# Kernel optimization log

Measured on AMD Instinct MI355X. Metric: run time of the kernel, lower is better.

## Reference

```python
import jax, jax.numpy as jnp
import numpy as np

D_MODEL = 128
SEQ_LEN = 2048
WINDOW = 64
BATCH = 32


def setup_inputs() -> dict:
    key = jax.random.key(0)
    ks = jax.random.split(key, 6)
    scale = 1.0 / np.sqrt(D_MODEL)
    return {
        "x": jax.random.normal(ks[0], (BATCH, D_MODEL, SEQ_LEN), dtype=jnp.float32),
        "Wq": jax.random.normal(ks[1], (D_MODEL, D_MODEL), dtype=jnp.float32) * scale,
        "bq": jnp.zeros((D_MODEL,), dtype=jnp.float32),
        "Wk": jax.random.normal(ks[2], (D_MODEL, D_MODEL), dtype=jnp.float32) * scale,
        "bk": jnp.zeros((D_MODEL,), dtype=jnp.float32),
        "Wv": jax.random.normal(ks[3], (D_MODEL, D_MODEL), dtype=jnp.float32) * scale,
        "bv": jnp.zeros((D_MODEL,), dtype=jnp.float32),
        "Wo": jax.random.normal(ks[4], (D_MODEL, D_MODEL), dtype=jnp.float32) * scale,
        "bo": jnp.zeros((D_MODEL,), dtype=jnp.float32),
        "pos_bias": jax.random.normal(ks[5], (SEQ_LEN, SEQ_LEN), dtype=jnp.float32) * 0.02,
    }


def reference(x, Wq, bq, Wk, bk, Wv, bv, Wo, bo, pos_bias):
    # x: [N, C, L] -> [N, L, C]  (in_proj Rearrange)
    xt = jnp.swapaxes(x, 1, 2)
    L = xt.shape[1]

    q = xt @ Wq + bq  # [N, L, d]
    k = xt @ Wk + bk
    v = xt @ Wv + bv

    # AFT-Local positional bias: w_{t,t'} = pos_bias if |t-t'| < s else 0
    idx = jnp.arange(L)
    local_mask = (jnp.abs(idx[:, None] - idx[None, :]) < WINDOW).astype(xt.dtype)
    pb = pos_bias[:L, :L] * local_mask  # [L, L]

    # numerically stable exponentials (AFT paper / labml formulation)
    exp_k = jnp.exp(k - jnp.max(k, axis=1, keepdims=True))          # [N, L, d]
    exp_pb = jnp.exp(pb - jnp.max(pb, axis=1, keepdims=True))       # [L, L]

    num = jnp.einsum('ij,njd->nid', exp_pb, exp_k * v)  # [N, L, d]
    den = jnp.einsum('ij,njd->nid', exp_pb, exp_k)      # [N, L, d]

    y = jax.nn.sigmoid(q) * num / den
    out = y @ Wo + bo  # output projection

    # out_proj Rearrange: [N, L, C] -> [N, C, L]
    return jnp.swapaxes(out, 1, 2)
```

## Files before the change

### kernel.cpp

```cpp
#include <hip/hip_runtime.h>
#include <hip/hip_bf16.h>
#include <math.h>

#define NB 32
#define DM 128
#define SL 2048
#define WIN 64
#define NT  (SL / 16)
#define PADF 4
#define PADB 6
#define NTP (NT + PADF + PADB)
#define YST 132
#define OST 68
#define NSEG 64

typedef __attribute__((ext_vector_type(8))) short bf16x8;
typedef __attribute__((ext_vector_type(8))) unsigned short u16x8;
typedef __attribute__((ext_vector_type(4))) float f32x4;
typedef __attribute__((ext_vector_type(4))) unsigned int u32x4;

__device__ inline ushort bf16_rne(float f) {
    union { float f; unsigned u; } v; v.f = f;
    unsigned u = v.u;
    return (ushort)((u + 0x7FFFu + ((u >> 16) & 1u)) >> 16);
}
__device__ inline float bf16_to_f(ushort h) {
    union { unsigned u; float f; } v; v.u = ((unsigned)h) << 16;
    return v.f;
}
__device__ inline unsigned pk_bf16(float a, float b) {
    union { __hip_bfloat162 h; unsigned u; } v;
    v.h = __float22bfloat162_rn(make_float2(a, b));
    return v.u;
}


__global__ __launch_bounds__(512) void setup_kernel(
    const float* __restrict__ Wq, const float* __restrict__ Wk,
    const float* __restrict__ Wv, const float* __restrict__ Wo,
    const float* __restrict__ pos_bias,
    ushort* __restrict__ Wh, ushort* __restrict__ Wl,
    ushort* __restrict__ WB)
{
    const int b = blockIdx.x;
    const int tid = threadIdx.x;
    if (b < 128) {
        const int id = b;
        const int mat = id >> 5;
        const int ct = (id & 31) >> 2, ks = id & 3;
        const int lane = tid >> 3, j = tid & 7;
        const int k = ks * 32 + (lane >> 4) * 8 + j;
        const int col = ct * 16 + (lane & 15);
        const float* W = (mat == 0) ? Wq : ((mat == 1) ? Wk : ((mat == 2) ? Wv : Wo));
        float w = W[k * DM + col];
        ushort h = bf16_rne(w);
        Wh[(size_t)id * 512 + tid] = h;
        Wl[(size_t)id * 512 + tid] = bf16_rne(w - bf16_to_f(h));
    } else {
        const int idx = b - 128;
        const int it = idx >> 1;
        const int half = idx & 1;
        const int i0 = it * 16;
        const int tend = half * 1280 + 1280;
        for (int t = half * 1280 + tid; t < tend; t += 512) {
            const int ks = t >> 9;
            const int lane = (t >> 3) & 63;
            const int jj = t & 7;
            const int m = lane & 15;
            const int k = ks * 32 + ((lane >> 4) << 3) + jj;
            const int i = i0 + m;
            const int j = i0 - 64 + k;
            const int rel = k - 64 - m;
            float val = 0.f;
            if (rel > -WIN && rel < WIN && j >= 0 && j < SL)
                val = __expf(pos_bias[(size_t)i * SL + j]) - 1.f;
            WB[(size_t)it * 2560 + t] = bf16_rne(val);
        }
    }
}

__global__ __launch_bounds__(512, 6) void qkv_kernel(
    const float* __restrict__ x,
    const ushort* __restrict__ Wh, const ushort* __restrict__ Wl,
    const float* __restrict__ bq, const float* __restrict__ bk,
    const float* __restrict__ bv,
    ushort* __restrict__ sqT, ushort* __restrict__ ekTF, ushort* __restrict__ ekvTF,
    float* __restrict__ Pk, float* __restrict__ Pkv)
{
    __shared__ ushort Ah[32 * 128];
    __shared__ ushort Al[32 * 128];
    const int n = blockIdx.y, bx = blockIdx.x, l0 = bx * 32;
    const int tid = threadIdx.x;
    const int wave = tid >> 6;
    const int lane = tid & 63;

    if (bx < 10) {
        const int jt_p = (bx < PADF) ? bx : (NT + bx);
        const size_t zb = ((size_t)n * NTP + jt_p) * 2048 + (size_t)tid * 4;
        ushort4 z; z.x = 0; z.y = 0; z.z = 0; z.w = 0;
        *(ushort4*)&ekTF [zb] = z;
        *(ushort4*)&ekvTF[zb] = z;
    }

    {
        const int lo = tid & 31;
        const int cq = tid >> 5;
        const int l  = l0 + lo;
        const int c0 = cq * 8;
        float xv[8];
        #pragma unroll
        for (int u = 0; u < 8; ++u)
            xv[u] = x[((size_t)n * DM + c0 + u) * SL + l];
        unsigned xb[8];
        #pragma unroll
        for (int u = 0; u < 8; ++u) xb[u] = __float_as_uint(xv[u]);
        unsigned hv32[4], lv32[4];
        #pragma unroll
        for (int p = 0; p < 4; ++p) {
            hv32[p] = (xb[2 * p] >> 16) | (xb[2 * p + 1] & 0xFFFF0000u);
            const float r0 = xv[2 * p]     - __uint_as_float(xb[2 * p]     & 0xFFFF0000u);
            const float r1 = xv[2 * p + 1] - __uint_as_float(xb[2 * p + 1] & 0xFFFF0000u);
            lv32[p] = pk_bf16(r0, r1);
        }
        const int lt = lo >> 4, m = lo & 15;
        const int ks = cq >> 2, oct = cq & 3;
        const int idx = ((lt * 4 + ks) * 64 + oct * 16 + m) * 8;
        *(uint4*)&Ah[idx] = make_uint4(hv32[0], hv32[1], hv32[2], hv32[3]);
        *(uint4*)&Al[idx] = make_uint4(lv32[0], lv32[1], lv32[2], lv32[3]);
    }
    __syncthreads();

    const int dcol = lane & 15;
    const int d = wave * 16 + dcol;

    f32x4 acc[3][2];
    {
        const float b0 = bq[d], b1 = bk[d], b2 = bv[d];
        #pragma unroll
        for (int lt = 0; lt < 2; ++lt) {
            acc[0][lt] = (f32x4){b0, b0, b0, b0};
            acc[1][lt] = (f32x4){b1, b1, b1, b1};
            acc[2][lt] = (f32x4){b2, b2, b2, b2};
        }
    }

    const bf16x8* WhV = (const bf16x8*)Wh;
    const bf16x8* WlV = (const bf16x8*)Wl;
    #pragma unroll
    for (int ks = 0; ks < 4; ++ks) {
        bf16x8 bh[3], bl[3];
        #pragma unroll
        for (int m = 0; m < 3; ++m) {
            const int fi = ((m * 8 + wave) * 4 + ks) * 64 + lane;
            bh[m] = WhV[fi];
            bl[m] = WlV[fi];
        }
        #pragma unroll
        for (int lt = 0; lt < 2; ++lt) {
            const bf16x8 ah = *(const bf16x8*)&Ah[((lt * 4 + ks) * 64 + lane) * 8];
            const bf16x8 al = *(const bf16x8*)&Al[((lt * 4 + ks) * 64 + lane) * 8];
            #pragma unroll
            for (int m = 0; m < 3; ++m) {
                acc[m][lt] = __builtin_amdgcn_mfma_f32_16x16x32_bf16(
                    ah, bh[m], acc[m][lt], 0, 0, 0);
                acc[m][lt] = __builtin_amdgcn_mfma_f32_16x16x32_bf16(
                    al, bh[m], acc[m][lt], 0, 0, 0);
                acc[m][lt] = __builtin_amdgcn_mfma_f32_16x16x32_bf16(
                    ah, bl[m], acc[m][lt], 0, 0, 0);
            }
        }
    }

    const int lrow0 = (lane >> 4) * 4;
    float psk = 0.f, pskv = 0.f;
    #pragma unroll
    for (int lt = 0; lt < 2; ++lt) {
        const f32x4 q4 = acc[0][lt];
        const f32x4 k4 = acc[1][lt];
        const f32x4 v4 = acc[2][lt];
        float e[4], z[4];
        unsigned su[4];
        #pragma unroll
        for (int r = 0; r < 4; ++r) {
            e[r] = __expf(k4[r]);
            z[r] = e[r] * v4[r];
            const float s = fminf(__builtin_amdgcn_rcpf(1.f + __expf(-q4[r])), 1.f);
            su[r] = (unsigned)(s * 65535.f + 0.5f);
            psk  += e[r];
            pskv += z[r];
        }
        const int jt = bx * 2 + lt;
        const size_t tb = ((size_t)n * NTP + PADF + jt) * 2048
                        + (size_t)d * 16 + lrow0;
        const size_t sb = ((size_t)n * NT + jt) * 2048
                        + (size_t)d * 16 + lrow0;
        *(uint2*)&ekTF [tb] = make_uint2(pk_bf16(e[0], e[1]), pk_bf16(e[2], e[3]));
        *(uint2*)&ekvTF[tb] = make_uint2(pk_bf16(z[0], z[1]), pk_bf16(z[2], z[3]));
        *(uint2*)&sqT  [sb] = make_uint2(su[0] | (su[1] << 16), su[2] | (su[3] << 16));
    }
    {
        float a = psk, b = pskv;
        a += __shfl_xor(a, 16, 64); a += __shfl_xor(a, 32, 64);
        b += __shfl_xor(b, 16, 64); b += __shfl_xor(b, 32, 64);
        if (lane < 16) {
            const size_t o = ((size_t)n * NSEG + bx) * DM + d;
            Pk [o] = a;
            Pkv[o] = b;
        }
    }
}

__global__ __launch_bounds__(256, 4) void band_out_kernel(
    const ushort* __restrict__ ekTF, const ushort* __restrict__ ekvTF,
    const ushort* __restrict__ WB,
    const float* __restrict__ Pk, const float* __restrict__ Pkv,
    const ushort* __restrict__ sqT,
    const ushort* __restrict__ Wh, const ushort* __restrict__ Wl,
    const float* __restrict__ bo, float* __restrict__ out)
{
    __shared__ __align__(16) union {
        float ylds[64 * YST];
        float ot[128 * OST];
        float red[8][DM];
    } u;
    __shared__ float SkL[DM], SkvL[DM];

    const int bid = blockIdx.x;
    const int xcd = bid & 7;
    const int slot = bid >> 3;
    const int nsub = slot >> 5;
    const int itg  = slot & 31;
    const int n = xcd * 4 + nsub;
    const int wave = threadIdx.x >> 6;
    const int lane = threadIdx.x & 63;
    const int it = itg * 4 + wave;
    const int l0 = itg * 64;

    const int dcol = lane & 15;
    const int jgrp8 = (lane >> 4) << 3;

    const bf16x8* WBv = (const bf16x8*)(WB + (size_t)it * 2560);
    bf16x8 aWB[5];
    #pragma unroll
    for (int ks = 0; ks < 5; ++ks) aWB[ks] = WBv[ks * 64 + lane];

    {
        const int tid = threadIdx.x;
        const int q = tid & 31;
        const int g = tid >> 5;
        const float* P = (g < 4) ? Pk : Pkv;
        const int s0 = (g & 3) * 16;
        f32x4 a4 = (f32x4){0.f, 0.f, 0.f, 0.f};
        #pragma unroll
        for (int s = 0; s < 16; ++s) {
            const f32x4 v = *(const f32x4*)&P[((size_t)n * NSEG + s0 + s) * DM + q * 4];
            a4 += v;
        }
        *(f32x4*)&u.red[g][q * 4] = a4;
    }
    __syncthreads();
    {
        const int tid = threadIdx.x;
        if (tid < 128)
            SkL[tid]  = u.red[0][tid] + u.red[1][tid] + u.red[2][tid] + u.red[3][tid];
        else {
            const int dd = tid - 128;
            SkvL[dd] = u.red[4][dd] + u.red[5][dd] + u.red[6][dd] + u.red[7][dd];
        }
    }
    __syncthreads();

    const size_t lsel = (size_t)(lane >> 5) * 2048 + (size_t)((lane >> 4) & 1) * 8
                      + (size_t)dcol * 16;
    size_t tb[5];
    #pragma unroll
    for (int ks = 0; ks < 5; ++ks)
        tb[ks] = ((size_t)n * NTP + it + 2 * ks) * 2048 + lsel;

    const int irow0 = (lane >> 4) << 2;
    const size_t sgb = ((size_t)n * NT + it) * 2048 + irow0;

    #pragma unroll
    for (int dt = 0; dt < 8; ++dt) {
        const int d = dt * 16 + dcol;
        const float sk = SkL[d];
        const float sv = SkvL[d];
        f32x4 den = (f32x4){sk, sk, sk, sk};
        f32x4 num = (f32x4){sv, sv, sv, sv};
        #pragma unroll
        for (int ks = 0; ks < 5; ++ks) {
            const size_t rbase = tb[ks] + (size_t)dt * 256;
            const bf16x8 bden = *(const bf16x8*)(ekTF  + rbase);
            const bf16x8 bnum = *(const bf16x8*)(ekvTF + rbase);
            den = __builtin_amdgcn_mfma_f32_16x16x32_bf16(aWB[ks], bden, den, 0, 0, 0);
            num = __builtin_amdgcn_mfma_f32_16x16x32_bf16(aWB[ks], bnum, num, 0, 0, 0);
        }
        const ushort4 s4 = *(const ushort4*)&sqT[sgb + (size_t)d * 16];
        float sf[4];
        sf[0] = (float)s4.x; sf[1] = (float)s4.y;
        sf[2] = (float)s4.z; sf[3] = (float)s4.w;
        #pragma unroll
        for (int r = 0; r < 4; ++r) {
            const float s = sf[r] * (1.f / 65535.f);
            const float y = s * num[r] * __builtin_amdgcn_rcpf(den[r]);
            u.ylds[(wave * 16 + irow0 + r) * YST + d] = y;
        }
    }

    bf16x8 yh[4], yl[4];
    {
        const int arow = wave * 16 + (lane & 15);
        #pragma unroll
        for (int ks = 0; ks < 4; ++ks) {
            const int base = arow * YST + ks * 32 + jgrp8;
            const float4 a0 = *(const float4*)&u.ylds[base];
            const float4 a1 = *(const float4*)&u.ylds[base + 4];
            float af[8];
            af[0] = a0.x; af[1] = a0.y; af[2] = a0.z; af[3] = a0.w;
            af[4] = a1.x; af[5] = a1.y; af[6] = a1.z; af[7] = a1.w;
            unsigned ab[8];
            #pragma unroll
            for (int t = 0; t < 8; ++t) ab[t] = __float_as_uint(af[t]);
            unsigned hw[4], lw[4];
            #pragma unroll
            for (int p = 0; p < 4; ++p) {
                hw[p] = (ab[2 * p] >> 16) | (ab[2 * p + 1] & 0xFFFF0000u);
                const float r0 = af[2 * p]     - __uint_as_float(ab[2 * p]     & 0xFFFF0000u);
                const float r1 = af[2 * p + 1] - __uint_as_float(ab[2 * p + 1] & 0xFFFF0000u);
                lw[p] = pk_bf16(r0, r1);
            }
            union { u32x4 w; bf16x8 b; } ch, cl;
            ch.w = (u32x4){hw[0], hw[1], hw[2], hw[3]};
            cl.w = (u32x4){lw[0], lw[1], lw[2], lw[3]};
            yh[ks] = ch.b;
            yl[ks] = cl.b;
        }
    }
    __syncthreads();

    const bf16x8* WhV = (const bf16x8*)Wh;
    const bf16x8* WlV = (const bf16x8*)Wl;
    #pragma unroll
    for (int ct = 0; ct < 8; ++ct) {
        const float b0 = bo[ct * 16 + dcol];
        f32x4 acc = (f32x4){b0, b0, b0, b0};
        #pragma unroll
        for (int ks = 0; ks < 4; ++ks) {
            const int fi = ((24 + ct) * 4 + ks) * 64 + lane;
            const bf16x8 bh = WhV[fi];
            const bf16x8 bl = WlV[fi];
            acc = __builtin_amdgcn_mfma_f32_16x16x32_bf16(yh[ks], bh, acc, 0, 0, 0);
            acc = __builtin_amdgcn_mfma_f32_16x16x32_bf16(yl[ks], bh, acc, 0, 0, 0);
            acc = __builtin_amdgcn_mfma_f32_16x16x32_bf16(yh[ks], bl, acc, 0, 0, 0);
        }
        const int c = ct * 16 + dcol;
        #pragma unroll
        for (int r = 0; r < 4; ++r)
            u.ot[c * OST + wave * 16 + irow0 + r] = acc[r];
    }
    __syncthreads();

    const int tid = threadIdx.x;
    #pragma unroll
    for (int rep = 0; rep < 8; ++rep) {
        const int e = rep * 256 + tid;
        const int c = e >> 4;
        const int lq = e & 15;
        const float4 v = *(const float4*)&u.ot[c * OST + lq * 4];
        *(float4*)&out[((size_t)n * DM + c) * SL + l0 + lq * 4] = v;
    }
}

extern "C" void kernel_launch(void* const* d_in, const int* in_sizes, int n_in,
                              void* d_out, int out_size, void* d_ws, size_t ws_size,
                              hipStream_t stream)
{
    const float* x        = (const float*)d_in[0];
    const float* Wq       = (const float*)d_in[1];
    const float* bq       = (const float*)d_in[2];
    const float* Wk       = (const float*)d_in[3];
    const float* bk       = (const float*)d_in[4];
    const float* Wv       = (const float*)d_in[5];
    const float* bv       = (const float*)d_in[6];
    const float* Wo       = (const float*)d_in[7];
    const float* bo       = (const float*)d_in[8];
    const float* pos_bias = (const float*)d_in[9];
    float* out = (float*)d_out;

    ushort* sqT   = (ushort*)d_ws;
    ushort* ekTF  = sqT   + (size_t)NB * NT * 2048;
    ushort* ekvTF = ekTF  + (size_t)NB * NTP * 2048;
    ushort* WB    = ekvTF + (size_t)NB * NTP * 2048;
    float*  Pk    = (float*)(WB + (size_t)128 * 2560);
    float*  Pkv   = Pk   + (size_t)NB * NSEG * DM;
    ushort* Wh    = (ushort*)(Pkv + (size_t)NB * NSEG * DM);
    ushort* Wl    = Wh + (size_t)4 * DM * DM;

    setup_kernel   <<<dim3(384),      512, 0, stream>>>(Wq, Wk, Wv, Wo, pos_bias,
                                                        Wh, Wl, WB);
    qkv_kernel     <<<dim3(NSEG, NB), 512, 0, stream>>>(x, Wh, Wl, bq, bk, bv,
                                                        sqT, ekTF, ekvTF, Pk, Pkv);
    band_out_kernel<<<dim3(NB * 32),  256, 0, stream>>>(ekTF, ekvTF, WB, Pk, Pkv, sqT,
                                                        Wh, Wl, bo, out);
}
```

Before: 155.8 us.

## Make QKV kernel persistent over 8 tiles with register-resident weights and double-buffered LDS

The QKV projection grid shrinks from 64x32 to 8x32 blocks, and each block loops over 8 sequence tiles. The Wq/Wk/Wv bf16 hi/lo fragments are loaded into registers once per block instead of once per tile. The next tile's x load is issued before the current tile's MFMAs, and its bf16 conversion goes into the other LDS buffer. This amortizes weight loads and hides global-load latency, but it uses many more registers (launch bounds drop to 1 block per SM) and cuts the grid to 256 blocks, which may underfill the GPU.

```diff
diff --git a/kernel.cpp b/kernel.cpp
--- a/kernel.cpp
+++ b/kernel.cpp
@@ -12,10 +12,10 @@
 #define NTP (NT + PADF + PADB)
 #define YST 132
 #define OST 68
-#define NSEG 64
+#define TPB 8
+#define QBX 8
 
 typedef __attribute__((ext_vector_type(8))) short bf16x8;
-typedef __attribute__((ext_vector_type(8))) unsigned short u16x8;
 typedef __attribute__((ext_vector_type(4))) float f32x4;
 typedef __attribute__((ext_vector_type(4))) unsigned int u32x4;
 
@@ -79,7 +79,7 @@
     }
 }
 
-__global__ __launch_bounds__(512, 6) void qkv_kernel(
+__global__ __launch_bounds__(512, 1) void qkv_kernel(
     const float* __restrict__ x,
     const ushort* __restrict__ Wh, const ushort* __restrict__ Wl,
     const float* __restrict__ bq, const float* __restrict__ bk,
@@ -87,30 +87,54 @@
     ushort* __restrict__ sqT, ushort* __restrict__ ekTF, ushort* __restrict__ ekvTF,
     float* __restrict__ Pk, float* __restrict__ Pkv)
 {
-    __shared__ ushort Ah[32 * 128];
-    __shared__ ushort Al[32 * 128];
-    const int n = blockIdx.y, bx = blockIdx.x, l0 = bx * 32;
+    __shared__ ushort Ah[2][32 * 128];
+    __shared__ ushort Al[2][32 * 128];
+    const int n = blockIdx.y, bx = blockIdx.x;
     const int tid = threadIdx.x;
     const int wave = tid >> 6;
     const int lane = tid & 63;
 
-    if (bx < 10) {
-        const int jt_p = (bx < PADF) ? bx : (NT + bx);
-        const size_t zb = ((size_t)n * NTP + jt_p) * 2048 + (size_t)tid * 4;
-        ushort4 z; z.x = 0; z.y = 0; z.z = 0; z.w = 0;
-        *(ushort4*)&ekTF [zb] = z;
-        *(ushort4*)&ekvTF[zb] = z;
-    }
-
-    {
-        const int lo = tid & 31;
-        const int cq = tid >> 5;
-        const int l  = l0 + lo;
-        const int c0 = cq * 8;
-        float xv[8];
+    {
+        const int nrep = (bx == 0) ? 3 : 1;
+        for (int s = 0; s < nrep; ++s) {
+            const int slot = (s == 0) ? bx : (7 + s);
+            const int jt_p = (slot < PADF) ? slot : (NT + slot);
+            const size_t zb = ((size_t)n * NTP + jt_p) * 2048 + (size_t)tid * 4;
+            ushort4 z; z.x = 0; z.y = 0; z.z = 0; z.w = 0;
+            *(ushort4*)&ekTF [zb] = z;
+            *(ushort4*)&ekvTF[zb] = z;
+        }
+    }
+
+    const bf16x8* WhV = (const bf16x8*)Wh;
+    const bf16x8* WlV = (const bf16x8*)Wl;
+    bf16x8 wfh[4][3], wfl[4][3];
+    #pragma unroll
+    for (int ks = 0; ks < 4; ++ks)
+        #pragma unroll
+        for (int m = 0; m < 3; ++m) {
+            const int fi = ((m * 8 + wave) * 4 + ks) * 64 + lane;
+            wfh[ks][m] = WhV[fi];
+            wfl[ks][m] = WlV[fi];
+        }
+
+    const int lo = tid & 31;
+    const int cq = tid >> 5;
+    const int c0 = cq * 8;
+    const int sidx = (((lo >> 4) * 4 + (cq >> 2)) * 64 + (cq & 3) * 16 + (lo & 15)) * 8;
+
+    const int dcol = lane & 15;
+    const int d = wave * 16 + dcol;
+    const float b0 = bq[d], b1 = bk[d], b2 = bv[d];
+    const int lrow0 = (lane >> 4) * 4;
+
+    auto LOADX = [&](int t, float* xv) {
+        const int l = (bx * TPB + t) * 32 + lo;
         #pragma unroll
         for (int u = 0; u < 8; ++u)
             xv[u] = x[((size_t)n * DM + c0 + u) * SL + l];
+    };
+    auto CVTWRITE = [&](const float* xv, int b) {
         unsigned xb[8];
         #pragma unroll
         for (int u = 0; u < 8; ++u) xb[u] = __float_as_uint(xv[u]);
@@ -122,88 +146,86 @@
             const float r1 = xv[2 * p + 1] - __uint_as_float(xb[2 * p + 1] & 0xFFFF0000u);
             lv32[p] = pk_bf16(r0, r1);
         }
-        const int lt = lo >> 4, m = lo & 15;
-        const int ks = cq >> 2, oct = cq & 3;
-        const int idx = ((lt * 4 + ks) * 64 + oct * 16 + m) * 8;
-        *(uint4*)&Ah[idx] = make_uint4(hv32[0], hv32[1], hv32[2], hv32[3]);
-        *(uint4*)&Al[idx] = make_uint4(lv32[0], lv32[1], lv32[2], lv32[3]);
+        *(uint4*)&Ah[b][sidx] = make_uint4(hv32[0], hv32[1], hv32[2], hv32[3]);
+        *(uint4*)&Al[b][sidx] = make_uint4(lv32[0], lv32[1], lv32[2], lv32[3]);
+    };
+
+    {
+        float xv[8];
+        LOADX(0, xv);
+        CVTWRITE(xv, 0);
     }
     __syncthreads();
 
-    const int dcol = lane & 15;
-    const int d = wave * 16 + dcol;
-
-    f32x4 acc[3][2];
-    {
-        const float b0 = bq[d], b1 = bk[d], b2 = bv[d];
+    float psk = 0.f, pskv = 0.f;
+    #pragma unroll
+    for (int t = 0; t < TPB; ++t) {
+        const int bsel = t & 1;
+        float xn[8];
+        if (t + 1 < TPB) LOADX(t + 1, xn);
+
+        f32x4 acc[3][2];
         #pragma unroll
         for (int lt = 0; lt < 2; ++lt) {
             acc[0][lt] = (f32x4){b0, b0, b0, b0};
             acc[1][lt] = (f32x4){b1, b1, b1, b1};
             acc[2][lt] = (f32x4){b2, b2, b2, b2};
         }
-    }
-
-    const bf16x8* WhV = (const bf16x8*)Wh;
-    const bf16x8* WlV = (const bf16x8*)Wl;
-    #pragma unroll
-    for (int ks = 0; ks < 4; ++ks) {
-        bf16x8 bh[3], bl[3];
-        #pragma unroll
-        for (int m = 0; m < 3; ++m) {
-            const int fi = ((m * 8 + wave) * 4 + ks) * 64 + lane;
-            bh[m] = WhV[fi];
-            bl[m] = WlV[fi];
-        }
+        #pragma unroll
+        for (int ks = 0; ks < 4; ++ks) {
+            #pragma unroll
+            for (int lt = 0; lt < 2; ++lt) {
+                const bf16x8 ah = *(const bf16x8*)&Ah[bsel][((lt * 4 + ks) * 64 + lane) * 8];
+                const bf16x8 al = *(const bf16x8*)&Al[bsel][((lt * 4 + ks) * 64 + lane) * 8];
+                #pragma unroll
+                for (int m = 0; m < 3; ++m) {
+                    acc[m][lt] = __builtin_amdgcn_mfma_f32_16x16x32_bf16(
+                        ah, wfh[ks][m], acc[m][lt], 0, 0, 0);
+                    acc[m][lt] = __builtin_amdgcn_mfma_f32_16x16x32_bf16(
+                        al, wfh[ks][m], acc[m][lt], 0, 0, 0);
+                    acc[m][lt] = __builtin_amdgcn_mfma_f32_16x16x32_bf16(
+                        ah, wfl[ks][m], acc[m][lt], 0, 0, 0);
+                }
+            }
+        }
+
+        const int gt = bx * TPB + t;
         #pragma unroll
         for (int lt = 0; lt < 2; ++lt) {
-            const bf16x8 ah = *(const bf16x8*)&Ah[((lt * 4 + ks) * 64 + lane) * 8];
-            const bf16x8 al = *(const bf16x8*)&Al[((lt * 4 + ks) * 64 + lane) * 8];
+            const f32x4 q4 = acc[0][lt];
+            const f32x4 k4 = acc[1][lt];
+            const f32x4 v4 = acc[2][lt];
+            float e[4], z[4];
+            unsigned su[4];
             #pragma unroll
-            for (int m = 0; m < 3; ++m) {
-                acc[m][lt] = __builtin_amdgcn_mfma_f32_16x16x32_bf16(
-                    ah, bh[m], acc[m][lt], 0, 0, 0);
-                acc[m][lt] = __builtin_amdgcn_mfma_f32_16x16x32_bf16(
-                    al, bh[m], acc[m][lt], 0, 0, 0);
-                acc[m][lt] = __builtin_amdgcn_mfma_f32_16x16x32_bf16(
-                    ah, bl[m], acc[m][lt], 0, 0, 0);
+            for (int r = 0; r < 4; ++r) {
+                e[r] = __expf(k4[r]);
+                z[r] = e[r] * v4[r];
+                const float s = fminf(__builtin_amdgcn_rcpf(1.f + __expf(-q4[r])), 1.f);
+                su[r] = (unsigned)(s * 65535.f + 0.5f);
+                psk  += e[r];
+                pskv += z[r];
             }
-        }
-    }
-
-    const int lrow0 = (lane >> 4) * 4;
-    float psk = 0.f, pskv = 0.f;
-    #pragma unroll
-    for (int lt = 0; lt < 2; ++lt) {
-        const f32x4 q4 = acc[0][lt];
-        const f32x4 k4 = acc[1][lt];
-        const f32x4 v4 = acc[2][lt];
-        float e[4], z[4];
-        unsigned su[4];
-        #pragma unroll
-        for (int r = 0; r < 4; ++r) {
-            e[r] = __expf(k4[r]);
-            z[r] = e[r] * v4[r];
-            const float s = fminf(__builtin_amdgcn_rcpf(1.f + __expf(-q4[r])), 1.f);
-            su[r] = (unsigned)(s * 65535.f + 0.5f);
-            psk  += e[r];
-            pskv += z[r];
-        }
-        const int jt = bx * 2 + lt;
-        const size_t tb = ((size_t)n * NTP + PADF + jt) * 2048
-                        + (size_t)d * 16 + lrow0;
-        const size_t sb = ((size_t)n * NT + jt) * 2048
-                        + (size_t)d * 16 + lrow0;
-        *(uint2*)&ekTF [tb] = make_uint2(pk_bf16(e[0], e[1]), pk_bf16(e[2], e[3]));
-        *(uint2*)&ekvTF[tb] = make_uint2(pk_bf16(z[0], z[1]), pk_bf16(z[2], z[3]));
-        *(uint2*)&sqT  [sb] = make_uint2(su[0] | (su[1] << 16), su[2] | (su[3] << 16));
-    }
+            const int jt = gt * 2 + lt;
+            const size_t tb = ((size_t)n * NTP + PADF + jt) * 2048
+                            + (size_t)d * 16 + lrow0;
+            const size_t sb = ((size_t)n * NT + jt) * 2048
+                            + (size_t)d * 16 + lrow0;
+            *(uint2*)&ekTF [tb] = make_uint2(pk_bf16(e[0], e[1]), pk_bf16(e[2], e[3]));
+            *(uint2*)&ekvTF[tb] = make_uint2(pk_bf16(z[0], z[1]), pk_bf16(z[2], z[3]));
+            *(uint2*)&sqT  [sb] = make_uint2(su[0] | (su[1] << 16), su[2] | (su[3] << 16));
+        }
+
+        if (t + 1 < TPB) CVTWRITE(xn, bsel ^ 1);
+        __syncthreads();
+    }
+
     {
         float a = psk, b = pskv;
         a += __shfl_xor(a, 16, 64); a += __shfl_xor(a, 32, 64);
         b += __shfl_xor(b, 16, 64); b += __shfl_xor(b, 32, 64);
         if (lane < 16) {
-            const size_t o = ((size_t)n * NSEG + bx) * DM + d;
+            const size_t o = ((size_t)n * QBX + bx) * DM + d;
             Pk [o] = a;
             Pkv[o] = b;
         }
@@ -249,11 +271,11 @@
         const int q = tid & 31;
         const int g = tid >> 5;
         const float* P = (g < 4) ? Pk : Pkv;
-        const int s0 = (g & 3) * 16;
+        const int s0 = (g & 3) * (QBX / 4);
         f32x4 a4 = (f32x4){0.f, 0.f, 0.f, 0.f};
         #pragma unroll
-        for (int s = 0; s < 16; ++s) {
-            const f32x4 v = *(const f32x4*)&P[((size_t)n * NSEG + s0 + s) * DM + q * 4];
+        for (int s = 0; s < QBX / 4; ++s) {
+            const f32x4 v = *(const f32x4*)&P[((size_t)n * QBX + s0 + s) * DM + q * 4];
             a4 += v;
         }
         *(f32x4*)&u.red[g][q * 4] = a4;
@@ -392,14 +414,14 @@
     ushort* ekvTF = ekTF  + (size_t)NB * NTP * 2048;
     ushort* WB    = ekvTF + (size_t)NB * NTP * 2048;
     float*  Pk    = (float*)(WB + (size_t)128 * 2560);
-    float*  Pkv   = Pk   + (size_t)NB * NSEG * DM;
-    ushort* Wh    = (ushort*)(Pkv + (size_t)NB * NSEG * DM);
+    float*  Pkv   = Pk   + (size_t)NB * QBX * DM;
+    ushort* Wh    = (ushort*)(Pkv + (size_t)NB * QBX * DM);
     ushort* Wl    = Wh + (size_t)4 * DM * DM;
 
-    setup_kernel   <<<dim3(384),      512, 0, stream>>>(Wq, Wk, Wv, Wo, pos_bias,
-                                                        Wh, Wl, WB);
-    qkv_kernel     <<<dim3(NSEG, NB), 512, 0, stream>>>(x, Wh, Wl, bq, bk, bv,
-                                                        sqT, ekTF, ekvTF, Pk, Pkv);
-    band_out_kernel<<<dim3(NB * 32),  256, 0, stream>>>(ekTF, ekvTF, WB, Pk, Pkv, sqT,
-                                                        Wh, Wl, bo, out);
-}
+    setup_kernel   <<<dim3(384),     512, 0, stream>>>(Wq, Wk, Wv, Wo, pos_bias,
+                                                       Wh, Wl, WB);
+    qkv_kernel     <<<dim3(QBX, NB), 512, 0, stream>>>(x, Wh, Wl, bq, bk, bv,
+                                                       sqT, ekTF, ekvTF, Pk, Pkv);
+    band_out_kernel<<<dim3(NB * 32), 256, 0, stream>>>(ekTF, ekvTF, WB, Pk, Pkv, sqT,
+                                                       Wh, Wl, bo, out);
+}
```

New measurement: 146.3 us, median of 2. 6.0% less time.
